# Kernel tuning notes

Measured on AMD Instinct MI355X. Metric: run time of the kernel, lower is better.

Reference implementation:

```python
import jax, jax.numpy as jnp
import numpy as np

VOCAB, EMB, H, D3, CTX = 30522, 768, 1024, 128, 512

def setup_inputs() -> dict:
    key = jax.random.key(0)
    ks = jax.random.split(key, 12)
    B, S = 8, 64
    inp = {
        'decoder_input_ids': jax.random.randint(ks[0], (B, S), 0, VOCAB, dtype=jnp.int64) if jax.config.jax_enable_x64 else jax.random.randint(ks[0], (B, S), 0, VOCAB, dtype=jnp.int32),
        'decoder_attn_mask': jnp.ones((B, S), dtype=jnp.int32),
        'decoder_seq_type_id': jnp.zeros((B, S), dtype=jnp.int32),
        'h_first': jax.random.normal(ks[1], (B, H), dtype=jnp.float32),
        'context': jax.random.normal(ks[2], (B, CTX, H), dtype=jnp.float32),
        # learned parameters (torch Linear stored transposed as [in, out])
        'emb_table': jax.random.normal(ks[3], (VOCAB, EMB), dtype=jnp.float32) * 0.02,
        'W_in': jax.random.normal(ks[4], (EMB, H), dtype=jnp.float32) * 0.02,
        'b_in': jnp.zeros((H,), dtype=jnp.float32),
        'W_s': jax.random.normal(ks[5], (H, H), dtype=jnp.float32) * 0.02,
        'b_s': jnp.zeros((H,), dtype=jnp.float32),
        'W_att_in': jax.random.normal(ks[6], (2 * H, D3), dtype=jnp.float32) * 0.02,
        'b_att_in': jnp.zeros((D3,), dtype=jnp.float32),
        'W_att_h': jax.random.normal(ks[7], (H, D3), dtype=jnp.float32) * 0.02,
        'b_att_h': jnp.zeros((D3,), dtype=jnp.float32),
        'V': jax.random.uniform(ks[8], (D3,), dtype=jnp.float32, minval=-1.0, maxval=1.0),
    }
    return inp


def reference(decoder_input_ids, decoder_attn_mask, decoder_seq_type_id, h_first,
              context, emb_table, W_in, b_in, W_s, b_s,
              W_att_in, b_att_in, W_att_h, b_att_h, V):
    # bert_embedding stub: plain token embedding lookup -> [B, S, 768]
    feats = emb_table[decoder_input_ids]
    # hidden_dense(context) is constant across steps; hoist it (same math)
    ctx_proj = context @ W_att_h + b_att_h          # [B, ctx, d3]
    h0 = context[:, -1, :]                          # initial recurrent state
    xs = jnp.swapaxes(feats, 0, 1)                  # [S, B, 768]

    def step(h, t_i):
        h = h @ W_s + b_s                           # dense_s
        s = jnp.concatenate([t_i @ W_in + b_in, h], axis=1)   # [B, 2H]
        a = jnp.tanh((s @ W_att_in + b_att_in)[:, None, :] + ctx_proj)  # [B,ctx,d3]
        att_before = jnp.einsum('d,bcd->bc', V, a)  # bmm(v, a^T) squeezed -> [B, ctx]
        # faithful to original: softmax over dim=1 of [B,1,ctx] (size-1 axis -> all ones)
        att_after = jax.nn.softmax(att_before[:, None, :], axis=1)[:, 0, :]
        idx = jnp.argmax(att_after, axis=1)         # ties -> 0, matches torch .max(1)
        return h, (att_before, idx)

    _, (atts, prts) = jax.lax.scan(step, h0, xs)
    atts = jnp.swapaxes(atts, 0, 1)                 # stack(dim=1).squeeze() -> [B, S, ctx]
    return atts, prts
```

## Files before the change

kernel.cpp:

```cpp
#include <hip/hip_runtime.h>
#include <hip/hip_bf16.h>

#define EMB 768
#define HD 1024
#define D3 128
#define CTXN 512
#define BB 8
#define SS 64

typedef __hip_bfloat16 bf16;
typedef __attribute__((ext_vector_type(8))) short short8v;
typedef __attribute__((ext_vector_type(4))) float f32x4;

__device__ __forceinline__ float fast_tanh(float x) {
  float e = __expf(2.f * x);
  return 1.f - 2.f * __builtin_amdgcn_rcpf(e + 1.f);
}

struct GDesc {
  const void* A;
  const bf16* BT;
  const int* arowmap;
  const float* addrow_f;
  const float* bias_f;
  float* Cf;
  bf16* Cb;
  bf16* CbT;
  float* brow_f;
  int M, N, K, lda, ldbt, ldct, af32, mtiles, blk0, nblks;
};
struct GBatch { GDesc d[10]; int nd; };

__global__ __launch_bounds__(256) void gemmz(GBatch bat) {
  int nwg = gridDim.x, orig = blockIdx.x;
  int q8 = nwg >> 3, r8 = nwg & 7;
  int xcd = orig & 7, idx = orig >> 3;
  int bx = (xcd < r8 ? xcd * (q8 + 1) : r8 * (q8 + 1) + (xcd - r8) * q8) + idx;

  GDesc d = bat.d[0];
  for (int i = 1; i < bat.nd; ++i)
    if (bx >= bat.d[i].blk0) d = bat.d[i];
  int local = bx - d.blk0;
  int mt = local % d.mtiles, nt = local / d.mtiles;
  int bm0 = mt * 32, bn0 = nt * 64;

  __shared__ bf16 As[2][32][128];
  __shared__ bf16 Bs[2][64][128];
  int tid = threadIdx.x, lane = tid & 63, wid = tid >> 6;
  int l16 = lane & 15, g = lane >> 4;
  int wm = (wid & 1) * 16, wn = (wid >> 1) * 32;
  int arow = tid >> 3, aseg = tid & 7;
  int brow = tid >> 2, bseg = tid & 3;
  f32x4 acc[2] = {};

  int agr = bm0 + arow;
  int asrc = (agr < d.M) ? (d.arowmap ? d.arowmap[agr] : agr) : -1;
  const float* Af = (const float*)d.A;
  const bf16* Ab = (const bf16*)d.A;

  float fa[16];
  short8v ba0 = {}, ba1 = {}, bb0 = {}, bb1 = {}, bb2 = {}, bb3 = {};
  int nk = d.K >> 7;

  auto LD = [&](int k0) {
    if (d.af32) {
      if (asrc >= 0) {
        const float* s = Af + (long)asrc * d.lda + k0 + aseg * 16;
#pragma unroll
        for (int j = 0; j < 16; ++j) fa[j] = s[j];
      } else {
#pragma unroll
        for (int j = 0; j < 16; ++j) fa[j] = 0.f;
      }
    } else {
      if (asrc >= 0) {
        const bf16* s = Ab + (long)asrc * d.lda + k0 + aseg * 16;
        ba0 = *(const short8v*)s;
        ba1 = *(const short8v*)(s + 8);
      } else {
        short8v z = {};
        ba0 = z; ba1 = z;
      }
    }
    const bf16* bsrc = d.BT + (long)(bn0 + brow) * d.ldbt + k0 + bseg * 32;
    bb0 = *(const short8v*)bsrc;
    bb1 = *(const short8v*)(bsrc + 8);
    bb2 = *(const short8v*)(bsrc + 16);
    bb3 = *(const short8v*)(bsrc + 24);
  };
  auto ST = [&](int buf) {
    int rs = arow & 7;
    if (d.af32) {
      bf16 t8[16];
#pragma unroll
      for (int j = 0; j < 16; ++j) t8[j] = __float2bfloat16(fa[j]);
      *(short8v*)&As[buf][arow][((2 * aseg) ^ rs) * 8] = *(short8v*)t8;
      *(short8v*)&As[buf][arow][((2 * aseg + 1) ^ rs) * 8] = *(short8v*)(t8 + 8);
    } else {
      *(short8v*)&As[buf][arow][((2 * aseg) ^ rs) * 8] = ba0;
      *(short8v*)&As[buf][arow][((2 * aseg + 1) ^ rs) * 8] = ba1;
    }
    int rb = brow & 7;
    *(short8v*)&Bs[buf][brow][((4 * bseg) ^ rb) * 8] = bb0;
    *(short8v*)&Bs[buf][brow][((4 * bseg + 1) ^ rb) * 8] = bb1;
    *(short8v*)&Bs[buf][brow][((4 * bseg + 2) ^ rb) * 8] = bb2;
    *(short8v*)&Bs[buf][brow][((4 * bseg + 3) ^ rb) * 8] = bb3;
  };

  LD(0);
  ST(0);
  __syncthreads();
  for (int it = 0; it < nk; ++it) {
    int cur = it & 1;
    if (it + 1 < nk) LD((it + 1) << 7);
    int ar = wm + l16;
    int ars = ar & 7;
#pragma unroll
    for (int kf = 0; kf < 4; ++kf) {
      short8v a = *(const short8v*)&As[cur][ar][((kf * 4 + g) ^ ars) * 8];
#pragma unroll
      for (int j = 0; j < 2; ++j) {
        int br = wn + j * 16 + l16;
        short8v b = *(const short8v*)&Bs[cur][br][((kf * 4 + g) ^ (br & 7)) * 8];
        acc[j] = __builtin_amdgcn_mfma_f32_16x16x32_bf16(a, b, acc[j], 0, 0, 0);
      }
    }
    if (it + 1 < nk) ST(cur ^ 1);
    __syncthreads();
  }

  float* Cs = (float*)&Bs[0][0][0];
  bool doT = (d.CbT != nullptr);
#pragma unroll
  for (int j = 0; j < 2; ++j)
#pragma unroll
    for (int r = 0; r < 4; ++r) {
      int gl = wm + g * 4 + r, cl = wn + j * 16 + l16;
      int grow = bm0 + gl, gcol = bn0 + cl;
      float v = acc[j][r];
      if (d.bias_f) v += d.bias_f[gcol];
      if (d.addrow_f && grow == d.M - 1) v += d.addrow_f[gcol];
      if (grow < d.M) {
        if (d.Cf) d.Cf[(long)grow * d.N + gcol] = v;
        if (d.Cb) d.Cb[(long)grow * d.N + gcol] = __float2bfloat16(v);
        if (d.brow_f && grow == d.M - 1) d.brow_f[gcol] = v;
      }
      if (doT) Cs[cl * 33 + gl] = v;
    }
  if (doT) {
    __syncthreads();
    int ctrows = d.M < 1024 ? d.M : 1024;
    int n = tid >> 2, ms = (tid & 3) * 8;
    int gm0 = bm0 + ms;
    bf16 t8[8];
#pragma unroll
    for (int jj = 0; jj < 8; ++jj) t8[jj] = __float2bfloat16(Cs[n * 33 + ms + jj]);
    if (gm0 + 7 < ctrows) {
      *(short8v*)&d.CbT[(long)(bn0 + n) * d.ldct + gm0] = *(short8v*)t8;
    } else {
#pragma unroll
      for (int jj = 0; jj < 8; ++jj)
        if (gm0 + jj < ctrows) d.CbT[(long)(bn0 + n) * d.ldct + gm0 + jj] = t8[jj];
    }
  }
}

__global__ __launch_bounds__(256) void kcast(const float* __restrict__ W_s,
                                             const float* __restrict__ b_s,
                                             const float* __restrict__ context,
                                             const float* __restrict__ b_in,
                                             const float* __restrict__ W_att_in,
                                             const float* __restrict__ b_att_in,
                                             const float* __restrict__ W_att_h,
                                             const int* __restrict__ ids,
                                             bf16* __restrict__ Mb0,
                                             bf16* __restrict__ Mb0T,
                                             bf16* __restrict__ Y0T,
                                             bf16* __restrict__ WahT,
                                             bf16* __restrict__ WaiT,
                                             bf16* __restrict__ Gb,
                                             float* __restrict__ qb,
                                             int* __restrict__ rowmap,
                                             bf16* __restrict__ ctxb) {
  int blk = blockIdx.x, tid = threadIdx.x;
  __shared__ bf16 tl[64][65];
  __shared__ float red[2][128];

  auto TP = [&](const float* src, int R, int C, bf16* dst, int tr, int tc) {
    int r0 = tr * 64, c0 = tc * 64;
    {
      int r = tid >> 2, cs = (tid & 3) * 16;
      const float* s = src + (long)(r0 + r) * C + c0 + cs;
#pragma unroll
      for (int j = 0; j < 16; ++j) tl[cs + j][r] = __float2bfloat16(s[j]);
    }
    __syncthreads();
    {
      int c = tid >> 2, rs = (tid & 3) * 16;
      bf16 o[16];
#pragma unroll
      for (int j = 0; j < 16; ++j) o[j] = tl[c][rs + j];
      *(short8v*)&dst[(long)(c0 + c) * R + r0 + rs] = *(short8v*)&o[0];
      *(short8v*)&dst[(long)(c0 + c) * R + r0 + rs + 8] = *(short8v*)&o[8];
    }
  };

  if (blk < 256) {
    long base = (long)blk * 4096;
    for (int i = tid; i < 4096; i += 256)
      Mb0[base + i] = __float2bfloat16(W_s[base + i]);
  } else if (blk == 256) {
    for (int i = tid; i < HD; i += 256)
      Mb0[(long)HD * HD + i] = __float2bfloat16(b_s[i]);
  } else if (blk < 513) {
    int t = blk - 257;
    TP(W_s, 1024, 1024, Mb0T, t >> 4, t & 15);
  } else if (blk < 545) {
    int t = blk - 513;
    TP(W_att_in + (long)1024 * D3, 1024, 128, Y0T, t >> 1, t & 1);
  } else if (blk < 577) {
    int t = blk - 545;
    TP(W_att_h, 1024, 128, WahT, t >> 1, t & 1);
  } else if (blk < 609) {
    int t = blk - 577;
    TP(W_att_in, 1024, 128, WaiT, t >> 1, t & 1);
  } else if (blk == 609) {
    for (int i = tid; i < BB * HD; i += 256) {
      int b = i >> 10, k = i & 1023;
      Gb[i] = __float2bfloat16(context[((long)b * CTXN + CTXN - 1) * HD + k]);
    }
  } else if (blk == 610) {
    int dd = tid & 127, h = tid >> 7;
    float acc = 0.f;
    for (int k = h * 512; k < h * 512 + 512; ++k)
      acc += b_in[k] * W_att_in[k * D3 + dd];
    red[h][dd] = acc;
    __syncthreads();
    if (h == 0) qb[dd] = red[0][dd] + red[1][dd] + b_att_in[dd];
  } else if (blk == 611) {
    for (int i = tid; i < 512; i += 256) {
      int t = i >> 3, b = i & 7;
      rowmap[i] = ids[b * SS + t];
    }
  } else {
    long base = (long)(blk - 612) * 4096;
    const float4* src = (const float4*)(context + base);
    int f0 = tid * 4;
    float4 v0 = src[f0], v1 = src[f0 + 1], v2 = src[f0 + 2], v3 = src[f0 + 3];
    bf16 o[16];
    o[0] = __float2bfloat16(v0.x); o[1] = __float2bfloat16(v0.y);
    o[2] = __float2bfloat16(v0.z); o[3] = __float2bfloat16(v0.w);
    o[4] = __float2bfloat16(v1.x); o[5] = __float2bfloat16(v1.y);
    o[6] = __float2bfloat16(v1.z); o[7] = __float2bfloat16(v1.w);
    o[8] = __float2bfloat16(v2.x); o[9] = __float2bfloat16(v2.y);
    o[10] = __float2bfloat16(v2.z); o[11] = __float2bfloat16(v2.w);
    o[12] = __float2bfloat16(v3.x); o[13] = __float2bfloat16(v3.y);
    o[14] = __float2bfloat16(v3.z); o[15] = __float2bfloat16(v3.w);
    *(short8v*)&ctxb[base + tid * 16] = *(short8v*)&o[0];
    *(short8v*)&ctxb[base + tid * 16 + 8] = *(short8v*)&o[8];
  }
}

__global__ __launch_bounds__(256) void katt(const float* __restrict__ qF,
                                            const float* __restrict__ qH,
                                            const float* __restrict__ ctxp,
                                            const float* __restrict__ V,
                                            float* __restrict__ out) {
  int blk = blockIdx.x;
  int b = blk >> 5, tt = (blk >> 4) & 1, ct = blk & 15;
  int t0 = tt * 32, c0 = ct * 32;
  int tid = threadIdx.x;
  __shared__ float lq[32][128];
  __shared__ float lc[32][132];
  __shared__ float lv[128];
  for (int i = tid; i < 32 * 128; i += 256) {
    int r = i >> 7, d = i & 127;
    int t = t0 + r;
    lq[r][d] = qF[((long)t * 8 + b) * 128 + d] +
               qH[(((long)(t & 7)) * 64 + (t >> 3) * 8 + b) * 128 + d];
    lc[r][d] = ctxp[((long)b * CTXN + c0 + r) * D3 + d];
  }
  if (tid < 128) lv[tid] = V[tid];
  __syncthreads();
  int cl = tid & 31, tg = tid >> 5;
  float r4[4] = {0.f, 0.f, 0.f, 0.f};
  for (int d4 = 0; d4 < 32; ++d4) {
    float4 cv = *reinterpret_cast<const float4*>(&lc[cl][d4 * 4]);
    float4 vv = *reinterpret_cast<const float4*>(&lv[d4 * 4]);
#pragma unroll
    for (int u = 0; u < 4; ++u) {
      int t = tg + u * 8;
      float4 qv = *reinterpret_cast<const float4*>(&lq[t][d4 * 4]);
      r4[u] = fmaf(vv.x, fast_tanh(qv.x + cv.x), r4[u]);
      r4[u] = fmaf(vv.y, fast_tanh(qv.y + cv.y), r4[u]);
      r4[u] = fmaf(vv.z, fast_tanh(qv.z + cv.z), r4[u]);
      r4[u] = fmaf(vv.w, fast_tanh(qv.w + cv.w), r4[u]);
    }
  }
#pragma unroll
  for (int u = 0; u < 4; ++u) {
    int t = tg + u * 8;
    out[((long)b * SS + (t0 + t)) * CTXN + c0 + cl] = r4[u];
  }
  if (blk == 0) {
    for (int i = tid; i < SS * BB; i += 256) out[(long)BB * SS * CTXN + i] = 0.f;
  }
}

static inline GDesc mk(const void* A, int af32, int lda, const int* arowmap,
                       const bf16* BT, int ldbt, int M, int N, int K,
                       const float* addrow_f, const float* bias_f, float* Cf,
                       bf16* Cb, bf16* CbT, int ldct, float* brow_f, int blk0) {
  GDesc d;
  d.A = A; d.BT = BT; d.arowmap = arowmap;
  d.addrow_f = addrow_f; d.bias_f = bias_f;
  d.Cf = Cf; d.Cb = Cb; d.CbT = CbT; d.brow_f = brow_f;
  d.M = M; d.N = N; d.K = K; d.lda = lda; d.ldbt = ldbt; d.ldct = ldct;
  d.af32 = af32;
  d.mtiles = (M + 31) >> 5;
  d.blk0 = blk0;
  d.nblks = d.mtiles * (N >> 6);
  return d;
}

extern "C" void kernel_launch(void* const* d_in, const int* in_sizes, int n_in,
                              void* d_out, int out_size, void* d_ws, size_t ws_size,
                              hipStream_t stream) {
  const int* ids = (const int*)d_in[0];
  const float* context = (const float*)d_in[4];
  const float* emb = (const float*)d_in[5];
  const float* W_in = (const float*)d_in[6];
  const float* b_in = (const float*)d_in[7];
  const float* W_s = (const float*)d_in[8];
  const float* b_s = (const float*)d_in[9];
  const float* W_att_in = (const float*)d_in[10];
  const float* b_att_in = (const float*)d_in[11];
  const float* W_att_h = (const float*)d_in[12];
  const float* b_att_h = (const float*)d_in[13];
  const float* V = (const float*)d_in[14];

  float* ws = (float*)d_ws;
  float* ctxp = ws;
  float* Yf = ctxp + 524288;
  float* qF = Yf + 1180800;
  float* qH = qF + 65536;
  float* qb = qH + 65536;
  float* brow2 = qb + 128;
  float* brow4 = brow2 + 1024;
  float* brow8 = brow4 + 1024;
  float* brow16 = brow8 + 1024;
  float* brow32 = brow16 + 1024;
  int* rowmap = (int*)(brow32 + 1024);
  bf16* bfp = (bf16*)(rowmap + 512);
  bf16* Mb0 = bfp;
  bf16* Mb0T = Mb0 + 1049600;
  bf16* Mb1 = Mb0T + 1048576;
  bf16* Mb1T = Mb1 + 1049600;
  bf16* Mb2 = Mb1T + 1048576;
  bf16* Mb2T = Mb2 + 1049600;
  bf16* Mb3 = Mb2T + 1048576;
  bf16* Mb3T = Mb3 + 1049600;
  bf16* YT = Mb3T + 1048576;
  bf16* WahT = YT + 9 * 131072;
  bf16* WaiT = WahT + 131072;
  bf16* WcT = WaiT + 131072;
  bf16* Gb = WcT + 131072;
  bf16* ctxb = Gb + 65536;
  float* out = (float*)d_out;

  auto Yfr = [&](int r) { return Yf + (long)r * 131200; };
  auto YTs = [&](int r) { return YT + (long)r * 131072; };

  kcast<<<dim3(1636), dim3(256), 0, stream>>>(W_s, b_s, context, b_in, W_att_in,
                                              b_att_in, W_att_h, ids, Mb0, Mb0T,
                                              YTs(0), WahT, WaiT, Gb, qb, rowmap,
                                              ctxb);
  {
    GBatch bt{}; int c = 0;
    bt.d[0] = mk(Mb0, 0, 1024, nullptr, Mb0T, 1024, 1025, 1024, 1024, b_s, nullptr, nullptr, Mb1, Mb1T, 1024, brow2, c); c += bt.d[0].nblks;
    bt.d[1] = mk(Mb0, 0, 1024, nullptr, YTs(0), 1024, 1025, 128, 1024, nullptr, nullptr, Yfr(1), nullptr, YTs(1), 1024, nullptr, c); c += bt.d[1].nblks;
    bt.d[2] = mk(ctxb, 0, 1024, nullptr, WahT, 1024, 4096, 128, 1024, nullptr, b_att_h, ctxp, nullptr, nullptr, 0, nullptr, c); c += bt.d[2].nblks;
    bt.d[3] = mk(W_in, 1, 1024, nullptr, WaiT, 1024, 768, 128, 1024, nullptr, nullptr, nullptr, nullptr, WcT, 768, nullptr, c); c += bt.d[3].nblks;
    bt.nd = 4;
    gemmz<<<dim3(c), dim3(256), 0, stream>>>(bt);
  }
  {
    GBatch bt{}; int c = 0;
    bt.d[0] = mk(Mb1, 0, 1024, nullptr, Mb1T, 1024, 1025, 1024, 1024, brow2, nullptr, nullptr, Mb2, Mb2T, 1024, brow4, c); c += bt.d[0].nblks;
    bt.d[1] = mk(Mb1, 0, 1024, nullptr, YTs(0), 1024, 1025, 128, 1024, nullptr, nullptr, Yfr(2), nullptr, YTs(2), 1024, nullptr, c); c += bt.d[1].nblks;
    bt.d[2] = mk(Mb1, 0, 1024, nullptr, YTs(1), 1024, 1025, 128, 1024, Yfr(1) + 131072, nullptr, Yfr(3), nullptr, YTs(3), 1024, nullptr, c); c += bt.d[2].nblks;
    bt.d[3] = mk(emb, 1, 768, rowmap, WcT, 768, 512, 128, 768, nullptr, qb, qF, nullptr, nullptr, 0, nullptr, c); c += bt.d[3].nblks;
    bt.nd = 4;
    gemmz<<<dim3(c), dim3(256), 0, stream>>>(bt);
  }
  {
    GBatch bt{}; int c = 0;
    bt.d[0] = mk(Mb2, 0, 1024, nullptr, Mb2T, 1024, 1025, 1024, 1024, brow4, nullptr, nullptr, Mb3, Mb3T, 1024, brow8, c); c += bt.d[0].nblks;
    for (int s = 0; s < 4; ++s) {
      bt.d[1 + s] = mk(Mb2, 0, 1024, nullptr, YTs(s), 1024, 1025, 128, 1024,
                       (s == 0) ? nullptr : (Yfr(s) + 131072), nullptr,
                       Yfr(4 + s), nullptr, YTs(4 + s), 1024, nullptr, c);
      c += bt.d[1 + s].nblks;
    }
    bt.nd = 5;
    gemmz<<<dim3(c), dim3(256), 0, stream>>>(bt);
  }
  {
    GBatch bt{}; int c = 0;
    bt.d[0] = mk(Mb3, 0, 1024, nullptr, Mb3T, 1024, 1025, 1024, 1024, brow8, nullptr, nullptr, Mb1, Mb1T, 1024, brow16, c); c += bt.d[0].nblks;
    bt.d[1] = mk(Mb3, 0, 1024, nullptr, YTs(0), 1024, 1025, 128, 1024, nullptr, nullptr, Yfr(8), nullptr, YTs(8), 1024, nullptr, c); c += bt.d[1].nblks;
    bt.d[2] = mk(Gb, 0, 1024, nullptr, Mb3T, 1024, 8, 1024, 1024, nullptr, brow8, nullptr, Gb + 8192, nullptr, 0, nullptr, c); c += bt.d[2].nblks;
    bt.nd = 3;
    gemmz<<<dim3(c), dim3(256), 0, stream>>>(bt);
  }
  {
    GBatch bt{}; int c = 0;
    bt.d[0] = mk(Mb1, 0, 1024, nullptr, Mb1T, 1024, 1025, 1024, 1024, brow16, nullptr, nullptr, Mb2, Mb2T, 1024, brow32, c); c += bt.d[0].nblks;
    bt.d[1] = mk(Gb, 0, 1024, nullptr, Mb1T, 1024, 16, 1024, 1024, nullptr, brow16, nullptr, Gb + 16384, nullptr, 0, nullptr, c); c += bt.d[1].nblks;
    bt.nd = 2;
    gemmz<<<dim3(c), dim3(256), 0, stream>>>(bt);
  }
  {
    GBatch bt{}; int c = 0;
    bt.d[0] = mk(Gb, 0, 1024, nullptr, Mb2T, 1024, 32, 1024, 1024, nullptr, brow32, nullptr, Gb + 32768, nullptr, 0, nullptr, c); c += bt.d[0].nblks;
    bt.nd = 1;
    gemmz<<<dim3(c), dim3(256), 0, stream>>>(bt);
  }
  {
    GBatch bt{}; int c = 0;
    for (int r = 1; r <= 8; ++r) {
      bt.d[r - 1] = mk(Gb, 0, 1024, nullptr, YTs(r), 1024, 64, 128, 1024, nullptr,
                       Yfr(r) + 131072, qH + (long)(r - 1) * 8192, nullptr, nullptr,
                       0, nullptr, c);
      c += bt.d[r - 1].nblks;
    }
    bt.nd = 8;
    gemmz<<<dim3(c), dim3(256), 0, stream>>>(bt);
  }
  katt<<<dim3(256), dim3(256), 0, stream>>>(qF, qH, ctxp, V, out);
}
```

Baseline: 156.8 us.

## Fuse attention tiles into gemm launches and split qH projections across stages

Removes the separate context bf16 cast pass: the context projection GEMM now reads fp32 context directly. The final qH projection over Gb is split into three row chunks (8, 24, 32 rows), each issued in an earlier launch as soon as its Gb rows exist. The attention/tanh kernel is folded into gemmz as extra blocks: the first half of time steps runs alongside the last qH chunk and the second half in a final launch. The XCD block remapping is dropped. The goal is fewer launches and less serial tail work, at the cost of a larger shared-memory footprint per gemmz block and an fp32 A-path for the big context GEMM.

```diff
diff --git a/kernel.cpp b/kernel.cpp
--- a/kernel.cpp
+++ b/kernel.cpp
@@ -29,13 +29,64 @@
   float* brow_f;
   int M, N, K, lda, ldbt, ldct, af32, mtiles, blk0, nblks;
 };
-struct GBatch { GDesc d[10]; int nd; };
+struct GBatch {
+  GDesc d[10]; int nd;
+  int katt0, katt_toff;
+  const float* qF; const float* qH; const float* ctxp; const float* V;
+  float* out;
+};
+
+__device__ void katt_tile(const GBatch& bat, int i, char* SM) {
+  auto lq = (float(*)[128])SM;
+  auto lc = (float(*)[132])(SM + 16384);
+  float* lv = (float*)(SM + 33792);
+  int tid = threadIdx.x;
+  int b = i >> 4, ct = i & 15, tt = bat.katt_toff;
+  int t0 = tt * 32, c0 = ct * 32;
+  for (int k = tid; k < 32 * 128; k += 256) {
+    int r = k >> 7, d = k & 127;
+    int t = t0 + r;
+    lq[r][d] = bat.qF[((long)t * 8 + b) * 128 + d] +
+               bat.qH[(((long)(t & 7)) * 64 + (t >> 3) * 8 + b) * 128 + d];
+    lc[r][d] = bat.ctxp[((long)b * CTXN + c0 + r) * D3 + d];
+  }
+  if (tid < 128) lv[tid] = bat.V[tid];
+  __syncthreads();
+  int cl = tid & 31, tg = tid >> 5;
+  float r4[4] = {0.f, 0.f, 0.f, 0.f};
+  for (int d4 = 0; d4 < 32; ++d4) {
+    float4 cv = *reinterpret_cast<const float4*>(&lc[cl][d4 * 4]);
+    float4 vv = *reinterpret_cast<const float4*>(&lv[d4 * 4]);
+#pragma unroll
+    for (int u = 0; u < 4; ++u) {
+      int t = tg + u * 8;
+      float4 qv = *reinterpret_cast<const float4*>(&lq[t][d4 * 4]);
+      r4[u] = fmaf(vv.x, fast_tanh(qv.x + cv.x), r4[u]);
+      r4[u] = fmaf(vv.y, fast_tanh(qv.y + cv.y), r4[u]);
+      r4[u] = fmaf(vv.z, fast_tanh(qv.z + cv.z), r4[u]);
+      r4[u] = fmaf(vv.w, fast_tanh(qv.w + cv.w), r4[u]);
+    }
+  }
+#pragma unroll
+  for (int u = 0; u < 4; ++u) {
+    int t = tg + u * 8;
+    bat.out[((long)b * SS + (t0 + t)) * CTXN + c0 + cl] = r4[u];
+  }
+  if (i == 0 && tt == 0) {
+    for (int k = tid; k < SS * BB; k += 256)
+      bat.out[(long)BB * SS * CTXN + k] = 0.f;
+  }
+}
 
 __global__ __launch_bounds__(256) void gemmz(GBatch bat) {
-  int nwg = gridDim.x, orig = blockIdx.x;
-  int q8 = nwg >> 3, r8 = nwg & 7;
-  int xcd = orig & 7, idx = orig >> 3;
-  int bx = (xcd < r8 ? xcd * (q8 + 1) : r8 * (q8 + 1) + (xcd - r8) * q8) + idx;
+  __shared__ __align__(16) char SM[49152];
+  int bx = blockIdx.x;
+  if (bx >= bat.katt0) {
+    katt_tile(bat, bx - bat.katt0, SM);
+    return;
+  }
+  auto As = (bf16(*)[32][128])SM;
+  auto Bs = (bf16(*)[64][128])(SM + 16384);
 
   GDesc d = bat.d[0];
   for (int i = 1; i < bat.nd; ++i)
@@ -44,8 +95,6 @@
   int mt = local % d.mtiles, nt = local / d.mtiles;
   int bm0 = mt * 32, bn0 = nt * 64;
 
-  __shared__ bf16 As[2][32][128];
-  __shared__ bf16 Bs[2][64][128];
   int tid = threadIdx.x, lane = tid & 63, wid = tid >> 6;
   int l16 = lane & 15, g = lane >> 4;
   int wm = (wid & 1) * 16, wn = (wid >> 1) * 32;
@@ -129,7 +178,7 @@
     __syncthreads();
   }
 
-  float* Cs = (float*)&Bs[0][0][0];
+  float* Cs = (float*)(SM + 16384);
   bool doT = (d.CbT != nullptr);
 #pragma unroll
   for (int j = 0; j < 2; ++j)
@@ -180,8 +229,7 @@
                                              bf16* __restrict__ WaiT,
                                              bf16* __restrict__ Gb,
                                              float* __restrict__ qb,
-                                             int* __restrict__ rowmap,
-                                             bf16* __restrict__ ctxb) {
+                                             int* __restrict__ rowmap) {
   int blk = blockIdx.x, tid = threadIdx.x;
   __shared__ bf16 tl[64][65];
   __shared__ float red[2][128];
@@ -237,73 +285,11 @@
     red[h][dd] = acc;
     __syncthreads();
     if (h == 0) qb[dd] = red[0][dd] + red[1][dd] + b_att_in[dd];
-  } else if (blk == 611) {
+  } else {
     for (int i = tid; i < 512; i += 256) {
       int t = i >> 3, b = i & 7;
       rowmap[i] = ids[b * SS + t];
     }
-  } else {
-    long base = (long)(blk - 612) * 4096;
-    const float4* src = (const float4*)(context + base);
-    int f0 = tid * 4;
-    float4 v0 = src[f0], v1 = src[f0 + 1], v2 = src[f0 + 2], v3 = src[f0 + 3];
-    bf16 o[16];
-    o[0] = __float2bfloat16(v0.x); o[1] = __float2bfloat16(v0.y);
-    o[2] = __float2bfloat16(v0.z); o[3] = __float2bfloat16(v0.w);
-    o[4] = __float2bfloat16(v1.x); o[5] = __float2bfloat16(v1.y);
-    o[6] = __float2bfloat16(v1.z); o[7] = __float2bfloat16(v1.w);
-    o[8] = __float2bfloat16(v2.x); o[9] = __float2bfloat16(v2.y);
-    o[10] = __float2bfloat16(v2.z); o[11] = __float2bfloat16(v2.w);
-    o[12] = __float2bfloat16(v3.x); o[13] = __float2bfloat16(v3.y);
-    o[14] = __float2bfloat16(v3.z); o[15] = __float2bfloat16(v3.w);
-    *(short8v*)&ctxb[base + tid * 16] = *(short8v*)&o[0];
-    *(short8v*)&ctxb[base + tid * 16 + 8] = *(short8v*)&o[8];
-  }
-}
-
-__global__ __launch_bounds__(256) void katt(const float* __restrict__ qF,
-                                            const float* __restrict__ qH,
-                                            const float* __restrict__ ctxp,
-                                            const float* __restrict__ V,
-                                            float* __restrict__ out) {
-  int blk = blockIdx.x;
-  int b = blk >> 5, tt = (blk >> 4) & 1, ct = blk & 15;
-  int t0 = tt * 32, c0 = ct * 32;
-  int tid = threadIdx.x;
-  __shared__ float lq[32][128];
-  __shared__ float lc[32][132];
-  __shared__ float lv[128];
-  for (int i = tid; i < 32 * 128; i += 256) {
-    int r = i >> 7, d = i & 127;
-    int t = t0 + r;
-    lq[r][d] = qF[((long)t * 8 + b) * 128 + d] +
-               qH[(((long)(t & 7)) * 64 + (t >> 3) * 8 + b) * 128 + d];
-    lc[r][d] = ctxp[((long)b * CTXN + c0 + r) * D3 + d];
-  }
-  if (tid < 128) lv[tid] = V[tid];
-  __syncthreads();
-  int cl = tid & 31, tg = tid >> 5;
-  float r4[4] = {0.f, 0.f, 0.f, 0.f};
-  for (int d4 = 0; d4 < 32; ++d4) {
-    float4 cv = *reinterpret_cast<const float4*>(&lc[cl][d4 * 4]);
-    float4 vv = *reinterpret_cast<const float4*>(&lv[d4 * 4]);
-#pragma unroll
-    for (int u = 0; u < 4; ++u) {
-      int t = tg + u * 8;
-      float4 qv = *reinterpret_cast<const float4*>(&lq[t][d4 * 4]);
-      r4[u] = fmaf(vv.x, fast_tanh(qv.x + cv.x), r4[u]);
-      r4[u] = fmaf(vv.y, fast_tanh(qv.y + cv.y), r4[u]);
-      r4[u] = fmaf(vv.z, fast_tanh(qv.z + cv.z), r4[u]);
-      r4[u] = fmaf(vv.w, fast_tanh(qv.w + cv.w), r4[u]);
-    }
-  }
-#pragma unroll
-  for (int u = 0; u < 4; ++u) {
-    int t = tg + u * 8;
-    out[((long)b * SS + (t0 + t)) * CTXN + c0 + cl] = r4[u];
-  }
-  if (blk == 0) {
-    for (int i = tid; i < SS * BB; i += 256) out[(long)BB * SS * CTXN + i] = 0.f;
   }
 }
 
@@ -365,23 +351,27 @@
   bf16* WaiT = WahT + 131072;
   bf16* WcT = WaiT + 131072;
   bf16* Gb = WcT + 131072;
-  bf16* ctxb = Gb + 65536;
   float* out = (float*)d_out;
 
   auto Yfr = [&](int r) { return Yf + (long)r * 131200; };
   auto YTs = [&](int r) { return YT + (long)r * 131072; };
-
-  kcast<<<dim3(1636), dim3(256), 0, stream>>>(W_s, b_s, context, b_in, W_att_in,
-                                              b_att_in, W_att_h, ids, Mb0, Mb0T,
-                                              YTs(0), WahT, WaiT, Gb, qb, rowmap,
-                                              ctxb);
+  const int NOKATT = 1 << 30;
+
+  auto setk = [&](GBatch& bt, int katt0, int toff) {
+    bt.katt0 = katt0; bt.katt_toff = toff;
+    bt.qF = qF; bt.qH = qH; bt.ctxp = ctxp; bt.V = V; bt.out = out;
+  };
+
+  kcast<<<dim3(612), dim3(256), 0, stream>>>(W_s, b_s, context, b_in, W_att_in,
+                                             b_att_in, W_att_h, ids, Mb0, Mb0T,
+                                             YTs(0), WahT, WaiT, Gb, qb, rowmap);
   {
     GBatch bt{}; int c = 0;
     bt.d[0] = mk(Mb0, 0, 1024, nullptr, Mb0T, 1024, 1025, 1024, 1024, b_s, nullptr, nullptr, Mb1, Mb1T, 1024, brow2, c); c += bt.d[0].nblks;
     bt.d[1] = mk(Mb0, 0, 1024, nullptr, YTs(0), 1024, 1025, 128, 1024, nullptr, nullptr, Yfr(1), nullptr, YTs(1), 1024, nullptr, c); c += bt.d[1].nblks;
-    bt.d[2] = mk(ctxb, 0, 1024, nullptr, WahT, 1024, 4096, 128, 1024, nullptr, b_att_h, ctxp, nullptr, nullptr, 0, nullptr, c); c += bt.d[2].nblks;
+    bt.d[2] = mk(context, 1, 1024, nullptr, WahT, 1024, 4096, 128, 1024, nullptr, b_att_h, ctxp, nullptr, nullptr, 0, nullptr, c); c += bt.d[2].nblks;
     bt.d[3] = mk(W_in, 1, 1024, nullptr, WaiT, 1024, 768, 128, 1024, nullptr, nullptr, nullptr, nullptr, WcT, 768, nullptr, c); c += bt.d[3].nblks;
-    bt.nd = 4;
+    bt.nd = 4; setk(bt, NOKATT, 0);
     gemmz<<<dim3(c), dim3(256), 0, stream>>>(bt);
   }
   {
@@ -390,7 +380,7 @@
     bt.d[1] = mk(Mb1, 0, 1024, nullptr, YTs(0), 1024, 1025, 128, 1024, nullptr, nullptr, Yfr(2), nullptr, YTs(2), 1024, nullptr, c); c += bt.d[1].nblks;
     bt.d[2] = mk(Mb1, 0, 1024, nullptr, YTs(1), 1024, 1025, 128, 1024, Yfr(1) + 131072, nullptr, Yfr(3), nullptr, YTs(3), 1024, nullptr, c); c += bt.d[2].nblks;
     bt.d[3] = mk(emb, 1, 768, rowmap, WcT, 768, 512, 128, 768, nullptr, qb, qF, nullptr, nullptr, 0, nullptr, c); c += bt.d[3].nblks;
-    bt.nd = 4;
+    bt.nd = 4; setk(bt, NOKATT, 0);
     gemmz<<<dim3(c), dim3(256), 0, stream>>>(bt);
   }
   {
@@ -402,7 +392,7 @@
                        Yfr(4 + s), nullptr, YTs(4 + s), 1024, nullptr, c);
       c += bt.d[1 + s].nblks;
     }
-    bt.nd = 5;
+    bt.nd = 5; setk(bt, NOKATT, 0);
     gemmz<<<dim3(c), dim3(256), 0, stream>>>(bt);
   }
   {
@@ -410,32 +400,49 @@
     bt.d[0] = mk(Mb3, 0, 1024, nullptr, Mb3T, 1024, 1025, 1024, 1024, brow8, nullptr, nullptr, Mb1, Mb1T, 1024, brow16, c); c += bt.d[0].nblks;
     bt.d[1] = mk(Mb3, 0, 1024, nullptr, YTs(0), 1024, 1025, 128, 1024, nullptr, nullptr, Yfr(8), nullptr, YTs(8), 1024, nullptr, c); c += bt.d[1].nblks;
     bt.d[2] = mk(Gb, 0, 1024, nullptr, Mb3T, 1024, 8, 1024, 1024, nullptr, brow8, nullptr, Gb + 8192, nullptr, 0, nullptr, c); c += bt.d[2].nblks;
-    bt.nd = 3;
+    bt.nd = 3; setk(bt, NOKATT, 0);
     gemmz<<<dim3(c), dim3(256), 0, stream>>>(bt);
   }
   {
     GBatch bt{}; int c = 0;
     bt.d[0] = mk(Mb1, 0, 1024, nullptr, Mb1T, 1024, 1025, 1024, 1024, brow16, nullptr, nullptr, Mb2, Mb2T, 1024, brow32, c); c += bt.d[0].nblks;
     bt.d[1] = mk(Gb, 0, 1024, nullptr, Mb1T, 1024, 16, 1024, 1024, nullptr, brow16, nullptr, Gb + 16384, nullptr, 0, nullptr, c); c += bt.d[1].nblks;
-    bt.nd = 2;
-    gemmz<<<dim3(c), dim3(256), 0, stream>>>(bt);
-  }
-  {
-    GBatch bt{}; int c = 0;
-    bt.d[0] = mk(Gb, 0, 1024, nullptr, Mb2T, 1024, 32, 1024, 1024, nullptr, brow32, nullptr, Gb + 32768, nullptr, 0, nullptr, c); c += bt.d[0].nblks;
-    bt.nd = 1;
-    gemmz<<<dim3(c), dim3(256), 0, stream>>>(bt);
-  }
-  {
-    GBatch bt{}; int c = 0;
     for (int r = 1; r <= 8; ++r) {
-      bt.d[r - 1] = mk(Gb, 0, 1024, nullptr, YTs(r), 1024, 64, 128, 1024, nullptr,
+      bt.d[1 + r] = mk(Gb, 0, 1024, nullptr, YTs(r), 1024, 8, 128, 1024, nullptr,
                        Yfr(r) + 131072, qH + (long)(r - 1) * 8192, nullptr, nullptr,
                        0, nullptr, c);
+      c += bt.d[1 + r].nblks;
+    }
+    bt.nd = 10; setk(bt, NOKATT, 0);
+    gemmz<<<dim3(c), dim3(256), 0, stream>>>(bt);
+  }
+  {
+    GBatch bt{}; int c = 0;
+    bt.d[0] = mk(Gb, 0, 1024, nullptr, Mb2T, 1024, 32, 1024, 1024, nullptr, brow32, nullptr, Gb + 32768, nullptr, 0, nullptr, c); c += bt.d[0].nblks;
+    for (int r = 1; r <= 8; ++r) {
+      bt.d[r] = mk(Gb + 8192, 0, 1024, nullptr, YTs(r), 1024, 24, 128, 1024, nullptr,
+                   Yfr(r) + 131072, qH + (long)(r - 1) * 8192 + 1024, nullptr,
+                   nullptr, 0, nullptr, c);
+      c += bt.d[r].nblks;
+    }
+    bt.nd = 9; setk(bt, NOKATT, 0);
+    gemmz<<<dim3(c), dim3(256), 0, stream>>>(bt);
+  }
+  {
+    GBatch bt{}; int c = 0;
+    for (int r = 1; r <= 8; ++r) {
+      bt.d[r - 1] = mk(Gb + 32768, 0, 1024, nullptr, YTs(r), 1024, 32, 128, 1024,
+                       nullptr, Yfr(r) + 131072,
+                       qH + (long)(r - 1) * 8192 + 4096, nullptr, nullptr, 0,
+                       nullptr, c);
       c += bt.d[r - 1].nblks;
     }
-    bt.nd = 8;
-    gemmz<<<dim3(c), dim3(256), 0, stream>>>(bt);
-  }
-  katt<<<dim3(256), dim3(256), 0, stream>>>(qF, qH, ctxp, V, out);
-}
+    bt.nd = 8; setk(bt, c, 0);
+    gemmz<<<dim3(c + 128), dim3(256), 0, stream>>>(bt);
+  }
+  {
+    GBatch bt{};
+    bt.nd = 0; setk(bt, 0, 1);
+    gemmz<<<dim3(128), dim3(256), 0, stream>>>(bt);
+  }
+}
```

Measured after the change: 160.6 us. +2.4%, slower.
